# Optimization experiments

Hardware: AMD Instinct MI355X
Metric: run time of the kernel (lower is better)

Reference implementation:

```python
import jax, jax.numpy as jnp
import numpy as np

E, H, I, T = 8, 1024, 4096, 8192  # experts, hidden, intermediate, total tokens


def setup_inputs() -> dict:
    key = jax.random.key(0)
    k1, k2, k3 = jax.random.split(key, 3)
    hiddens = jax.random.normal(k1, (T, H), dtype=jnp.float32)
    # expert weights, scaled like standard init
    w1_weight = jax.random.normal(k2, (E, H, I), dtype=jnp.float32) * (1.0 / np.sqrt(H).astype(np.float32))
    w2_weight = jax.random.normal(k3, (E, I, H), dtype=jnp.float32) * (1.0 / np.sqrt(I).astype(np.float32))
    # tokens are pre-grouped by expert; equal load of T//E tokens per expert
    batch_sizes = jnp.full((E,), T // E, dtype=jnp.int32)
    return {"hiddens": hiddens, "batch_sizes": batch_sizes,
            "w1_weight": w1_weight, "w2_weight": w2_weight}


def _gmm(x, w, batch_sizes):
    """Grouped matmul: rows of x are grouped contiguously by expert.
    x: [T, K], w: [E, K, N], batch_sizes: [E] (sums to T). Returns [T, N].
    Loop is over the small fixed expert count; each iteration is a dense
    GEMM with rows outside the expert's segment masked to zero.
    """
    n_experts = w.shape[0]
    ends = jnp.cumsum(batch_sizes)
    starts = ends - batch_sizes
    tok = jnp.arange(x.shape[0])[:, None]  # [T, 1]
    out = jnp.zeros((x.shape[0], w.shape[2]), dtype=x.dtype)
    for e in range(n_experts):
        mask = (tok >= starts[e]) & (tok < ends[e])  # [T, 1]
        out = out + jnp.where(mask, x, jnp.zeros((), x.dtype)) @ w[e]
    return out


def reference(hiddens, batch_sizes, w1_weight, w2_weight):
    up = _gmm(hiddens, w1_weight, batch_sizes)    # [T, I]
    down = _gmm(up, w2_weight, batch_sizes)       # [T, H]
    return down
```

## Files before the change

### kernel.cpp

```cpp
#include <hip/hip_runtime.h>
#include <hip/hip_bf16.h>


typedef unsigned short u16;
typedef unsigned int u32;
typedef __attribute__((ext_vector_type(8))) short bf16x8;
typedef __attribute__((ext_vector_type(4))) float f32x4;
typedef __attribute__((ext_vector_type(4))) u32 u32x4;

#define E_N 8
#define H_N 1024
#define I_N 4096
#define T_N 8192

#define GLD2LDS16(g, l)                                                        \
  __builtin_amdgcn_global_load_lds(                                            \
      (const __attribute__((address_space(1))) void*)(g),                      \
      (__attribute__((address_space(3))) void*)(l), 16, 0, 0)

__device__ __forceinline__ u32 pkbf(float lo, float hi) {
  u32 a = __float_as_uint(lo) + 0x8000u;
  u32 b = __float_as_uint(hi) + 0x8000u;
  return __builtin_amdgcn_perm(b, a, 0x07060302u);
}

__device__ __forceinline__ u16 f2bf(float f) {
  __hip_bfloat16 h = __float2bfloat16(f);
  return *(reinterpret_cast<u16*>(&h));
}

__device__ __forceinline__ f32x4 ntload4(const float* p) {
  return __builtin_nontemporal_load((const f32x4*)p);
}

__device__ __forceinline__ int xcd_swz(int bid, int nwg) {
  const int chunk = nwg >> 3;
  return (bid & 7) * chunk + (bid >> 3);
}

#define NB_W1 16384
#define NB_X 4096
#define NB_TR 8192

__global__ __launch_bounds__(256) void prepass_kernel(
    const float* __restrict__ w1, const float* __restrict__ x,
    const float* __restrict__ w2, u16* __restrict__ w1b,
    u16* __restrict__ xb, u16* __restrict__ w2t) {
  __shared__ float tile[64 * 65];
  const int tid = threadIdx.x;
  const int bid = blockIdx.x;

  if (bid < NB_W1 + NB_X) {
    const float* src;
    u16* dst;
    size_t base;
    if (bid < NB_W1) {
      src = w1; dst = w1b; base = (size_t)bid * 2048;
    } else {
      src = x; dst = xb; base = (size_t)(bid - NB_W1) * 2048;
    }
    const size_t i = base + (size_t)tid * 8;
    f32x4 a = ntload4(src + i);
    f32x4 b = ntload4(src + i + 4);
    *(u32x4*)(dst + i) = (u32x4){pkbf(a.x, a.y), pkbf(a.z, a.w),
                                 pkbf(b.x, b.y), pkbf(b.z, b.w)};
    return;
  }

  const int b = bid - (NB_W1 + NB_X);
  const int e = b >> 10;
  const int rem = b & 1023;
  const int i0 = (rem >> 4) * 64;
  const int h0 = (rem & 15) * 64;
  const float* src = w2 + (size_t)e * I_N * H_N;
  u16* dst = w2t + (size_t)e * H_N * I_N;

  {
    const int r = tid >> 4;
    const int c4 = (tid & 15) * 4;
#pragma unroll
    for (int rr = 0; rr < 4; rr++) {
      const int row = rr * 16 + r;
      f32x4 v = ntload4(src + (size_t)(i0 + row) * H_N + h0 + c4);
      tile[row * 65 + c4 + 0] = v.x;
      tile[row * 65 + c4 + 1] = v.y;
      tile[row * 65 + c4 + 2] = v.z;
      tile[row * 65 + c4 + 3] = v.w;
    }
  }
  __syncthreads();

  {
    const int hr = tid >> 3;
    const int ic = (tid & 7) * 8;
#pragma unroll
    for (int hh = 0; hh < 2; hh++) {
      const int h = hh * 32 + hr;
      u32 p[4];
#pragma unroll
      for (int j = 0; j < 4; j++)
        p[j] = pkbf(tile[(ic + 2 * j) * 65 + h], tile[(ic + 2 * j + 1) * 65 + h]);
      *(u32x4*)(dst + (size_t)(h0 + h) * I_N + i0 + ic) =
          (u32x4){p[0], p[1], p[2], p[3]};
    }
  }
}

__global__ __launch_bounds__(256) void wgemm_kernel(const u16* __restrict__ w2t,
                                                    const u16* __restrict__ w1b,
                                                    u16* __restrict__ mt) {
  __shared__ u16 ldsA[4096];
  __shared__ u16 ldsB[4096];

  const int tid = threadIdx.x;
  const int lane = tid & 63;
  const int wv = tid >> 6;
  const int wm = wv >> 1, wn = wv & 1;
  const int lm = lane & 15, quad = lane >> 4;

  const int sbid = xcd_swz(blockIdx.x, 512);
  const int e = sbid >> 6;
  const int t = sbid & 63;
  const int row0 = (t >> 3) * 128;
  const int col0 = (t & 7) * 128;

  const u16* Ae = w2t + (size_t)e * H_N * I_N;
  const u16* Be = w1b + (size_t)e * H_N * I_N;
  u16* mte = mt + (size_t)e * H_N * H_N;

  const int s_r = tid >> 2;
  const int s_k = (tid & 3) * 8;
  const u16* gA0 = Ae + (size_t)(row0 + s_r) * I_N + s_k;
  const u16* gA1 = gA0 + (size_t)64 * I_N;
  const u16* gB0 = Be + (size_t)(col0 + s_r) * I_N + s_k;
  const u16* gB1 = gB0 + (size_t)64 * I_N;
  u16* ldsA_dst = ldsA + wv * 512;
  u16* ldsB_dst = ldsB + wv * 512;

  f32x4 acc[4][4];
#pragma unroll
  for (int i = 0; i < 4; i++)
#pragma unroll
    for (int j = 0; j < 4; j++) acc[i][j] = (f32x4){0.f, 0.f, 0.f, 0.f};

  for (int k0 = 0; k0 < I_N; k0 += 32) {
    GLD2LDS16(gA0 + k0, ldsA_dst);
    GLD2LDS16(gA1 + k0, ldsA_dst + 2048);
    GLD2LDS16(gB0 + k0, ldsB_dst);
    GLD2LDS16(gB1 + k0, ldsB_dst + 2048);

    __syncthreads();

    bf16x8 af[4], bfr[4];
#pragma unroll
    for (int mi = 0; mi < 4; mi++)
      af[mi] = *(const bf16x8*)(ldsA + (wm * 64 + mi * 16 + lm) * 32 + quad * 8);
#pragma unroll
    for (int ni = 0; ni < 4; ni++)
      bfr[ni] = *(const bf16x8*)(ldsB + (wn * 64 + ni * 16 + lm) * 32 + quad * 8);
#pragma unroll
    for (int mi = 0; mi < 4; mi++)
#pragma unroll
      for (int ni = 0; ni < 4; ni++)
        acc[mi][ni] = __builtin_amdgcn_mfma_f32_16x16x32_bf16(
            af[mi], bfr[ni], acc[mi][ni], 0, 0, 0);

    __syncthreads();
  }

  const int orow = row0 + wm * 64 + quad * 4;
  const int ocol = col0 + wn * 64 + lm;
#pragma unroll
  for (int mi = 0; mi < 4; mi++)
#pragma unroll
    for (int ni = 0; ni < 4; ni++)
#pragma unroll
      for (int r = 0; r < 4; r++)
        mte[(size_t)(orow + mi * 16 + r) * H_N + ocol + ni * 16] =
            f2bf(acc[mi][ni][r]);
}

template <int KSPLIT>
__global__ __launch_bounds__(256) void wgemm_split_kernel(
    const u16* __restrict__ w2t, const u16* __restrict__ w1b,
    float* __restrict__ mtp) {
  __shared__ u16 ldsA[4096];
  __shared__ u16 ldsB[4096];

  const int tid = threadIdx.x;
  const int lane = tid & 63;
  const int wv = tid >> 6;
  const int wm = wv >> 1, wn = wv & 1;
  const int lm = lane & 15, quad = lane >> 4;

  const int sbid = xcd_swz(blockIdx.x, 512 * KSPLIT);
  const int kh = sbid >> 9;
  const int bi = sbid & 511;
  const int e = bi >> 6;
  const int t = bi & 63;
  const int row0 = (t >> 3) * 128;
  const int col0 = (t & 7) * 128;

  const u16* Ae = w2t + (size_t)e * H_N * I_N;
  const u16* Be = w1b + (size_t)e * H_N * I_N;

  const int s_r = tid >> 2;
  const int s_k = (tid & 3) * 8;
  const u16* gA0 = Ae + (size_t)(row0 + s_r) * I_N + s_k;
  const u16* gA1 = gA0 + (size_t)64 * I_N;
  const u16* gB0 = Be + (size_t)(col0 + s_r) * I_N + s_k;
  const u16* gB1 = gB0 + (size_t)64 * I_N;
  u16* ldsA_dst = ldsA + wv * 512;
  u16* ldsB_dst = ldsB + wv * 512;

  f32x4 acc[4][4];
#pragma unroll
  for (int i = 0; i < 4; i++)
#pragma unroll
    for (int j = 0; j < 4; j++) acc[i][j] = (f32x4){0.f, 0.f, 0.f, 0.f};

  const int KSEG = I_N / KSPLIT;
  const int kbeg = kh * KSEG;
  for (int k0 = kbeg; k0 < kbeg + KSEG; k0 += 32) {
    GLD2LDS16(gA0 + k0, ldsA_dst);
    GLD2LDS16(gA1 + k0, ldsA_dst + 2048);
    GLD2LDS16(gB0 + k0, ldsB_dst);
    GLD2LDS16(gB1 + k0, ldsB_dst + 2048);

    __syncthreads();

    bf16x8 af[4], bfr[4];
#pragma unroll
    for (int mi = 0; mi < 4; mi++)
      af[mi] = *(const bf16x8*)(ldsA + (wm * 64 + mi * 16 + lm) * 32 + quad * 8);
#pragma unroll
    for (int ni = 0; ni < 4; ni++)
      bfr[ni] = *(const bf16x8*)(ldsB + (wn * 64 + ni * 16 + lm) * 32 + quad * 8);
#pragma unroll
    for (int mi = 0; mi < 4; mi++)
#pragma unroll
      for (int ni = 0; ni < 4; ni++)
        acc[mi][ni] = __builtin_amdgcn_mfma_f32_16x16x32_bf16(
            af[mi], bfr[ni], acc[mi][ni], 0, 0, 0);

    __syncthreads();
  }

  float* dst = mtp + ((size_t)(kh * E_N + e)) * H_N * H_N;
  const int orow = row0 + wm * 64 + quad * 4;
  const int ocol = col0 + wn * 64 + lm;
#pragma unroll
  for (int mi = 0; mi < 4; mi++)
#pragma unroll
    for (int ni = 0; ni < 4; ni++)
#pragma unroll
      for (int r = 0; r < 4; r++)
        __builtin_nontemporal_store(
            acc[mi][ni][r],
            dst + (size_t)(orow + mi * 16 + r) * H_N + ocol + ni * 16);
}

template <int KSPLIT>
__global__ __launch_bounds__(256) void reduce_mt_kernel(
    const float* __restrict__ mtp, u16* __restrict__ mt) {
  const size_t i = ((size_t)blockIdx.x * 256 + threadIdx.x) * 8;
  float s[8];
#pragma unroll
  for (int j = 0; j < 8; j++) s[j] = 0.f;
#pragma unroll
  for (int p = 0; p < KSPLIT; p++) {
    const float* q = mtp + (size_t)p * E_N * H_N * H_N + i;
    f32x4 a = ntload4(q);
    f32x4 b = ntload4(q + 4);
    s[0] += a.x; s[1] += a.y; s[2] += a.z; s[3] += a.w;
    s[4] += b.x; s[5] += b.y; s[6] += b.z; s[7] += b.w;
  }
  *(u32x4*)(mt + i) = (u32x4){pkbf(s[0], s[1]), pkbf(s[2], s[3]),
                              pkbf(s[4], s[5]), pkbf(s[6], s[7])};
}

__global__ __launch_bounds__(256) void tgemm_kernel(const u16* __restrict__ xb,
                                                    const int* __restrict__ bsz,
                                                    const u16* __restrict__ mt,
                                                    float* __restrict__ out) {
  __shared__ u16 ldsA[2048];
  __shared__ u16 ldsB[4096];

  const int tid = threadIdx.x;
  const int lane = tid & 63;
  const int wv = tid >> 6;
  const int wm = wv >> 1, wn = wv & 1;
  const int lm = lane & 15, quad = lane >> 4;

  const int sbid = xcd_swz(blockIdx.x, 1024);
  const int bm = sbid >> 3, bn = sbid & 7;
  const int row0 = bm * 64;
  const int col0 = bn * 128;

  int e = 0, start = 0;
#pragma unroll
  for (int i = 0; i < E_N; i++) {
    int b = bsz[i];
    if (row0 >= start + b) { start += b; e = i + 1; }
  }
  const u16* mte = mt + (size_t)e * H_N * H_N;

  const int s_r = tid >> 2;
  const int s_k = (tid & 3) * 8;
  const u16* gA0 = xb + (size_t)(row0 + s_r) * H_N + s_k;
  const u16* gB0 = mte + (size_t)(col0 + s_r) * H_N + s_k;
  const u16* gB1 = gB0 + (size_t)64 * H_N;
  u16* ldsA_dst = ldsA + wv * 512;
  u16* ldsB_dst = ldsB + wv * 512;

  f32x4 acc[2][4];
#pragma unroll
  for (int i = 0; i < 2; i++)
#pragma unroll
    for (int j = 0; j < 4; j++) acc[i][j] = (f32x4){0.f, 0.f, 0.f, 0.f};

  for (int k0 = 0; k0 < H_N; k0 += 32) {
    GLD2LDS16(gA0 + k0, ldsA_dst);
    GLD2LDS16(gB0 + k0, ldsB_dst);
    GLD2LDS16(gB1 + k0, ldsB_dst + 2048);

    __syncthreads();

    bf16x8 af[2], bfr[4];
#pragma unroll
    for (int mi = 0; mi < 2; mi++)
      af[mi] = *(const bf16x8*)(ldsA + (wm * 32 + mi * 16 + lm) * 32 + quad * 8);
#pragma unroll
    for (int ni = 0; ni < 4; ni++)
      bfr[ni] = *(const bf16x8*)(ldsB + (wn * 64 + ni * 16 + lm) * 32 + quad * 8);
#pragma unroll
    for (int mi = 0; mi < 2; mi++)
#pragma unroll
      for (int ni = 0; ni < 4; ni++)
        acc[mi][ni] = __builtin_amdgcn_mfma_f32_16x16x32_bf16(
            af[mi], bfr[ni], acc[mi][ni], 0, 0, 0);

    __syncthreads();
  }

  const int orow = row0 + wm * 32 + quad * 4;
  const int ocol = col0 + wn * 64 + lm;
#pragma unroll
  for (int mi = 0; mi < 2; mi++)
#pragma unroll
    for (int ni = 0; ni < 4; ni++)
#pragma unroll
      for (int r = 0; r < 4; r++)
        __builtin_nontemporal_store(
            acc[mi][ni][r],
            out + (size_t)(orow + mi * 16 + r) * H_N + ocol + ni * 16);
}

extern "C" void kernel_launch(void* const* d_in, const int* in_sizes, int n_in,
                              void* d_out, int out_size, void* d_ws,
                              size_t ws_size, hipStream_t stream) {
  (void)in_sizes; (void)n_in; (void)out_size;
  const float* hiddens = (const float*)d_in[0];
  const int* bsz = (const int*)d_in[1];
  const float* w1 = (const float*)d_in[2];
  const float* w2 = (const float*)d_in[3];
  float* out = (float*)d_out;

  char* ws = (char*)d_ws;
  u16* w1b = (u16*)(ws);
  u16* w2t = (u16*)(ws + (size_t)64 * 1024 * 1024);
  u16* xb  = (u16*)(ws + (size_t)128 * 1024 * 1024);
  u16* mt  = (u16*)(ws + (size_t)144 * 1024 * 1024);
  float* mtp = (float*)(ws + (size_t)160 * 1024 * 1024);
  const size_t MiB = 1024 * 1024;
  const int ksplit = (ws_size >= 288 * MiB) ? 4 : (ws_size >= 224 * MiB ? 2 : 1);

  prepass_kernel<<<dim3(NB_W1 + NB_X + NB_TR), 256, 0, stream>>>(
      w1, hiddens, w2, w1b, xb, w2t);

  if (ksplit == 4) {
    wgemm_split_kernel<4><<<dim3(2048), 256, 0, stream>>>(w2t, w1b, mtp);
    reduce_mt_kernel<4><<<dim3(4096), 256, 0, stream>>>(mtp, mt);
  } else if (ksplit == 2) {
    wgemm_split_kernel<2><<<dim3(1024), 256, 0, stream>>>(w2t, w1b, mtp);
    reduce_mt_kernel<2><<<dim3(4096), 256, 0, stream>>>(mtp, mt);
  } else {
    wgemm_kernel<<<dim3(512), 256, 0, stream>>>(w2t, w1b, mt);
  }

  tgemm_kernel<<<dim3(1024), 256, 0, stream>>>(xb, bsz, mt, out);
}
```

Baseline: 463.2 us.

## Replace split-K weight GEMM with 256x256 double-buffered swizzled LDS kernel

Replaces the 128x128 split-K weight-product GEMM with a 512-thread kernel that computes 256x256 tiles over K=64 steps, fixes split-K at 2, and keeps two LDS buffers so the next tile's global-to-LDS loads overlap the current tile's MFMAs. LDS rows are XOR-swizzled to avoid bank conflicts, and MFMA sections are raised to higher wave priority. The aim is to cut global traffic per FLOP and hide load latency, in exchange for heavy LDS use (128 KB per block) and more accumulator registers, which may limit occupancy. The grid shrinks to 256 blocks, so whether the CUs are filled is a concern.

```diff
diff --git a/kernel.cpp b/kernel.cpp
--- a/kernel.cpp
+++ b/kernel.cpp
@@ -180,77 +180,107 @@
             f2bf(acc[mi][ni][r]);
 }
 
-template <int KSPLIT>
-__global__ __launch_bounds__(256) void wgemm_split_kernel(
+__global__ __launch_bounds__(512, 2) void wgemm8_kernel(
     const u16* __restrict__ w2t, const u16* __restrict__ w1b,
     float* __restrict__ mtp) {
-  __shared__ u16 ldsA[4096];
-  __shared__ u16 ldsB[4096];
+  __shared__ u16 lds[65536];
 
   const int tid = threadIdx.x;
   const int lane = tid & 63;
   const int wv = tid >> 6;
-  const int wm = wv >> 1, wn = wv & 1;
+  const int wm = wv >> 2;
+  const int wn = wv & 3;
   const int lm = lane & 15, quad = lane >> 4;
 
-  const int sbid = xcd_swz(blockIdx.x, 512 * KSPLIT);
-  const int kh = sbid >> 9;
-  const int bi = sbid & 511;
-  const int e = bi >> 6;
-  const int t = bi & 63;
-  const int row0 = (t >> 3) * 128;
-  const int col0 = (t & 7) * 128;
+  const int sbid = xcd_swz(blockIdx.x, 256);
+  const int kh = sbid >> 7;
+  const int rem = sbid & 127;
+  const int e = rem >> 4;
+  const int t = rem & 15;
+  const int row0 = (t >> 2) * 256;
+  const int col0 = (t & 3) * 256;
 
   const u16* Ae = w2t + (size_t)e * H_N * I_N;
   const u16* Be = w1b + (size_t)e * H_N * I_N;
 
-  const int s_r = tid >> 2;
-  const int s_k = (tid & 3) * 8;
-  const u16* gA0 = Ae + (size_t)(row0 + s_r) * I_N + s_k;
-  const u16* gA1 = gA0 + (size_t)64 * I_N;
-  const u16* gB0 = Be + (size_t)(col0 + s_r) * I_N + s_k;
-  const u16* gB1 = gB0 + (size_t)64 * I_N;
-  u16* ldsA_dst = ldsA + wv * 512;
-  u16* ldsB_dst = ldsB + wv * 512;
-
-  f32x4 acc[4][4];
-#pragma unroll
-  for (int i = 0; i < 4; i++)
+  const int srow = tid >> 3;
+  const int koff = ((tid & 7) ^ (srow & 7)) * 8;
+  const u16* gA = Ae + (size_t)(row0 + srow) * I_N + koff;
+  const u16* gB = Be + (size_t)(col0 + srow) * I_N + koff;
+  u16* stA = lds + wv * 512;
+  u16* stB = stA + 16384;
+
+  const int sw = (lm & 7) << 4;
+  const int c0 = (((quad << 4)) ^ sw) >> 1;
+  const int c1 = ((64 | (quad << 4)) ^ sw) >> 1;
+  const int rdA = (wm * 128 + lm) * 64;
+  const int rdB = (wn * 64 + lm) * 64;
+
+  f32x4 acc[8][4];
+#pragma unroll
+  for (int i = 0; i < 8; i++)
 #pragma unroll
     for (int j = 0; j < 4; j++) acc[i][j] = (f32x4){0.f, 0.f, 0.f, 0.f};
 
-  const int KSEG = I_N / KSPLIT;
-  const int kbeg = kh * KSEG;
-  for (int k0 = kbeg; k0 < kbeg + KSEG; k0 += 32) {
-    GLD2LDS16(gA0 + k0, ldsA_dst);
-    GLD2LDS16(gA1 + k0, ldsA_dst + 2048);
-    GLD2LDS16(gB0 + k0, ldsB_dst);
-    GLD2LDS16(gB1 + k0, ldsB_dst + 2048);
-
-    __syncthreads();
-
-    bf16x8 af[4], bfr[4];
-#pragma unroll
-    for (int mi = 0; mi < 4; mi++)
-      af[mi] = *(const bf16x8*)(ldsA + (wm * 64 + mi * 16 + lm) * 32 + quad * 8);
-#pragma unroll
-    for (int ni = 0; ni < 4; ni++)
-      bfr[ni] = *(const bf16x8*)(ldsB + (wn * 64 + ni * 16 + lm) * 32 + quad * 8);
-#pragma unroll
-    for (int mi = 0; mi < 4; mi++)
+  const int kbeg = kh * (I_N / 2);
+  const int NT = (I_N / 2) / 64;
+
+#define STAGE8(bsel, k0)                                                       \
+  do {                                                                         \
+    u16* la = stA + (bsel)*32768;                                              \
+    u16* lb = stB + (bsel)*32768;                                              \
+    const u16* ga = gA + (k0);                                                 \
+    const u16* gb = gB + (k0);                                                 \
+    GLD2LDS16(ga, la);                                                         \
+    GLD2LDS16(ga + (size_t)64 * I_N, la + 4096);                               \
+    GLD2LDS16(ga + (size_t)128 * I_N, la + 8192);                              \
+    GLD2LDS16(ga + (size_t)192 * I_N, la + 12288);                             \
+    GLD2LDS16(gb, lb);                                                         \
+    GLD2LDS16(gb + (size_t)64 * I_N, lb + 4096);                               \
+    GLD2LDS16(gb + (size_t)128 * I_N, lb + 8192);                              \
+    GLD2LDS16(gb + (size_t)192 * I_N, lb + 12288);                             \
+  } while (0)
+
+  STAGE8(0, kbeg);
+  for (int kt = 0; kt < NT; ++kt) {
+    if (kt + 1 < NT) {
+      STAGE8((kt + 1) & 1, kbeg + (kt + 1) * 64);
+      asm volatile("s_waitcnt vmcnt(8)" ::: "memory");
+    } else {
+      asm volatile("s_waitcnt vmcnt(0)" ::: "memory");
+    }
+    asm volatile("s_barrier" ::: "memory");
+
+    const u16* bufA = lds + (kt & 1) * 32768;
+    const u16* bufB = bufA + 16384;
+#pragma unroll
+    for (int kh2 = 0; kh2 < 2; ++kh2) {
+      const int cc = kh2 ? c1 : c0;
+      bf16x8 a[8], b[4];
 #pragma unroll
       for (int ni = 0; ni < 4; ni++)
-        acc[mi][ni] = __builtin_amdgcn_mfma_f32_16x16x32_bf16(
-            af[mi], bfr[ni], acc[mi][ni], 0, 0, 0);
-
-    __syncthreads();
-  }
-
-  float* dst = mtp + ((size_t)(kh * E_N + e)) * H_N * H_N;
-  const int orow = row0 + wm * 64 + quad * 4;
+        b[ni] = *(const bf16x8*)(bufB + rdB + ni * 1024 + cc);
+#pragma unroll
+      for (int mi = 0; mi < 8; mi++)
+        a[mi] = *(const bf16x8*)(bufA + rdA + mi * 1024 + cc);
+      __builtin_amdgcn_s_setprio(1);
+#pragma unroll
+      for (int mi = 0; mi < 8; mi++)
+#pragma unroll
+        for (int ni = 0; ni < 4; ni++)
+          acc[mi][ni] = __builtin_amdgcn_mfma_f32_16x16x32_bf16(
+              a[mi], b[ni], acc[mi][ni], 0, 0, 0);
+      __builtin_amdgcn_s_setprio(0);
+    }
+    asm volatile("s_barrier" ::: "memory");
+  }
+#undef STAGE8
+
+  float* dst = mtp + (size_t)(kh * E_N + e) * H_N * H_N;
+  const int orow = row0 + wm * 128 + quad * 4;
   const int ocol = col0 + wn * 64 + lm;
 #pragma unroll
-  for (int mi = 0; mi < 4; mi++)
+  for (int mi = 0; mi < 8; mi++)
 #pragma unroll
     for (int ni = 0; ni < 4; ni++)
 #pragma unroll
@@ -373,16 +403,12 @@
   u16* mt  = (u16*)(ws + (size_t)144 * 1024 * 1024);
   float* mtp = (float*)(ws + (size_t)160 * 1024 * 1024);
   const size_t MiB = 1024 * 1024;
-  const int ksplit = (ws_size >= 288 * MiB) ? 4 : (ws_size >= 224 * MiB ? 2 : 1);
 
   prepass_kernel<<<dim3(NB_W1 + NB_X + NB_TR), 256, 0, stream>>>(
       w1, hiddens, w2, w1b, xb, w2t);
 
-  if (ksplit == 4) {
-    wgemm_split_kernel<4><<<dim3(2048), 256, 0, stream>>>(w2t, w1b, mtp);
-    reduce_mt_kernel<4><<<dim3(4096), 256, 0, stream>>>(mtp, mt);
-  } else if (ksplit == 2) {
-    wgemm_split_kernel<2><<<dim3(1024), 256, 0, stream>>>(w2t, w1b, mtp);
+  if (ws_size >= 224 * MiB) {
+    wgemm8_kernel<<<dim3(256), 512, 0, stream>>>(w2t, w1b, mtp);
     reduce_mt_kernel<2><<<dim3(4096), 256, 0, stream>>>(mtp, mt);
   } else {
     wgemm_kernel<<<dim3(512), 256, 0, stream>>>(w2t, w1b, mt);
```

After: 410.1 us. 11.5% less time.
